# Kernel optimization log

Hardware: AMD Instinct MI355X
Metric: run time of the kernel (lower is better)

The kernel has to match this reference:

```python
import jax, jax.numpy as jnp
import numpy as np

N = 8192          # number of candidate boxes
NUM_CLASSES = 80  # COCO-style class count
IOU_THRESHOLD = 0.45


def setup_inputs() -> dict:
    key = jax.random.key(0)
    k1, k2, k3, k4 = jax.random.split(key, 4)
    # valid xyxy boxes: top-left in [0,1000), width/height in [1,101)
    xy = jax.random.uniform(k1, (N, 2)) * 1000.0
    wh = jax.random.uniform(k2, (N, 2)) * 100.0 + 1.0
    boxes = jnp.concatenate([xy, xy + wh], axis=1)            # [N,4]
    scores = jax.random.uniform(k3, (N,))                     # [N], all > 0
    idxs = jax.random.randint(k4, (N,), 0, NUM_CLASSES)       # [N] class ids
    return {"boxes": boxes, "scores": scores, "idxs": idxs}


def _nms_keep_mask(boxes, scores, iou_thr):
    """Greedy NMS (torchvision semantics) on a single set of boxes.
    Returns a boolean keep mask in the ORIGINAL box order."""
    n = boxes.shape[0]
    order = jnp.argsort(-scores)          # score-descending priority
    b = boxes[order]                      # [n,4]
    area = (b[:, 2] - b[:, 0]) * (b[:, 3] - b[:, 1])
    lt = jnp.maximum(b[:, None, :2], b[None, :, :2])   # [n,n,2]
    rb = jnp.minimum(b[:, None, 2:], b[None, :, 2:])   # [n,n,2]
    wh = jnp.clip(rb - lt, 0.0)
    inter = wh[..., 0] * wh[..., 1]                    # [n,n]
    iou = inter / (area[:, None] + area[None, :] - inter)
    over = iou > iou_thr                               # [n,n] bool
    lower_priority = jnp.arange(n)

    def body(i, suppressed):
        kept_i = jnp.logical_not(suppressed[i])
        # a kept box suppresses all lower-priority boxes it overlaps too much
        return suppressed | (kept_i & over[i] & (lower_priority > i))

    suppressed = jax.lax.fori_loop(0, n, body, jnp.zeros((n,), bool))
    # scatter keep decisions back to original order
    return jnp.zeros((n,), bool).at[order].set(~suppressed)


def reference(boxes, scores, idxs):
    iou_threshold = IOU_THRESHOLD
    # per-class coordinate offsets make boxes of different classes disjoint,
    # so one global NMS == the per-class NMS loop of the torch module
    max_coordinate = boxes.max()
    offsets = idxs.astype(boxes.dtype) * (max_coordinate + 1.0)
    boxes_for_nms = boxes + offsets[:, None]
    keep_mask = _nms_keep_mask(boxes_for_nms, scores, iou_threshold)
    # suppressed boxes get score 0 (all real scores are > 0), so after the
    # descending sort the kept boxes occupy the leading rows exactly as in
    # the torch module; suppressed boxes pad the tail (fixed output shape).
    scores_after_nms = jnp.where(keep_mask, scores, 0.0)
    inds = jnp.argsort(-scores_after_nms)      # [N] keep indices, score-desc
    sorted_scores = scores_after_nms[inds]
    out_boxes = jnp.concatenate([boxes[inds], sorted_scores[:, None]], axis=-1)
    return (out_boxes, inds)
```

## Files before the change

### kernel.cpp

```cpp
#include <hip/hip_runtime.h>
#include <stdint.h>

#define NBOX 8192
#define NW   128
#define IOU_THR 0.45f
#define NCLS 80
#define SEGCAP 128
#define CLSCAP 256
#define EDGE_LDS 2048
#define TAIL_BLOCKS 8

typedef unsigned long long u64;
typedef unsigned int u32;
typedef unsigned short u16;

__global__ void __launch_bounds__(256) k_pm(const float4* __restrict__ boxes4,
                                            const int* __restrict__ idxs,
                                            const float* __restrict__ scores,
                                            u32* __restrict__ ent,
                                            u32* __restrict__ entCnt,
                                            u16* __restrict__ rank16g) {
    int b = blockIdx.x, t = threadIdx.x;
    if (b < NCLS) {
        __shared__ float4 lb[CLSCAP];
        __shared__ float  la[CLSCAP];
        __shared__ float  ls[CLSCAP];
        __shared__ int    lj[CLSCAP];
        __shared__ float  red[256];
        __shared__ u32    ccnt, lcnt;
        float mx = 0.0f;
        for (int i = t; i < NBOX; i += 256) {
            float4 v = boxes4[i];
            mx = fmaxf(mx, fmaxf(fmaxf(v.x, v.y), fmaxf(v.z, v.w)));
        }
        red[t] = mx;
        __syncthreads();
        for (int s = 128; s > 0; s >>= 1) {
            if (t < s) red[t] = fmaxf(red[t], red[t + s]);
            __syncthreads();
        }
        float mc1 = red[0] + 1.0f;
        float off = (float)b * mc1;
        if (t == 0) { ccnt = 0; lcnt = 0; }
        __syncthreads();
        for (int j = t; j < NBOX; j += 256) {
            if (idxs[j] == b) {
                u32 x = atomicAdd(&ccnt, 1u);
                if (x < CLSCAP) {
                    float4 bx = boxes4[j];
                    bx.x += off; bx.y += off; bx.z += off; bx.w += off;
                    lb[x] = bx;
                    la[x] = (bx.z - bx.x) * (bx.w - bx.y);
                    ls[x] = scores[j];
                    lj[x] = j;
                }
            }
        }
        __syncthreads();
        u32 cnt = min(ccnt, (u32)CLSCAP);
        if ((u32)t < cnt) {
            float4 bv = lb[t];
            float  av = la[t];
            float  sv = ls[t];
            int    jv = lj[t];
            for (u32 u = 0; u < (u32)t; ++u) {
                float4 bu = lb[u];
                float ltx = fmaxf(bu.x, bv.x), lty = fmaxf(bu.y, bv.y);
                float rbx = fminf(bu.z, bv.z), rby = fminf(bu.w, bv.w);
                float wx = fmaxf(rbx - ltx, 0.0f), wy = fmaxf(rby - lty, 0.0f);
                float inter = wx * wy;
                if (inter > 0.0f) {
                    float iou = inter / (la[u] + av - inter);
                    if (iou > IOU_THR) {
                        float su = ls[u];
                        int   iu = lj[u];
                        bool uwin = (su > sv) || (su == sv && iu < jv);
                        u32 winI  = uwin ? (u32)iu : (u32)jv;
                        u32 loseI = uwin ? (u32)jv : (u32)iu;
                        u32 x = atomicAdd(&lcnt, 1u);
                        if (x < SEGCAP) ent[b * SEGCAP + x] = (loseI << 13) | winI;
                    }
                }
            }
        }
        __syncthreads();
        if (t == 0) entCnt[b] = min(lcnt, (u32)SEGCAP);
    } else {
        __shared__ u64 lk[2048];
        __shared__ u16 part[256];
        int rb = b - NCLS;
        int jj = rb * 32 + (t & 31);
        u64 kj = ((u64)(~__float_as_uint(scores[jj])) << 32) | (u32)jj;
        int cnt = 0;
        int p = t >> 5;
        for (int ch = 0; ch < 4; ++ch) {
            for (int i = t; i < 2048; i += 256) {
                int g = ch * 2048 + i;
                lk[i] = ((u64)(~__float_as_uint(scores[g])) << 32) | (u32)g;
            }
            __syncthreads();
            int base = p * 256;
#pragma unroll 8
            for (int i = 0; i < 256; ++i) cnt += (lk[base + i] < kj) ? 1 : 0;
            __syncthreads();
        }
        part[t] = (u16)cnt;
        __syncthreads();
        if (t < 32) {
            int s = 0;
#pragma unroll
            for (int q = 0; q < 8; ++q) s += part[q * 32 + t];
            rank16g[rb * 32 + t] = (u16)s;
        }
    }
}

__global__ void __launch_bounds__(1024)
k_tail(const u32* __restrict__ ent, const u32* __restrict__ entCnt,
       const u16* __restrict__ rank16g, const float4* __restrict__ boxes4,
       const float* __restrict__ scores, float* __restrict__ out) {
    __shared__ u32 sedge[EDGE_LDS];
    __shared__ u16 rank16[NBOX];
    __shared__ u32 scnt[NCLS];
    __shared__ u64 kw[NW], sup[NW], kws[NW];
    __shared__ u32 wps[NW], wpo[NW];
    __shared__ u32 s_m, s_nk;
    __shared__ int chg;

    int t = threadIdx.x;
    if (t < NCLS) scnt[t] = entCnt[t];
    for (int j = t; j < NBOX; j += 1024) rank16[j] = rank16g[j];
    if (t < NW) { kw[t] = ~0ULL; kws[t] = 0ULL; }
    if (t == 0) s_m = 0;
    __syncthreads();
    for (u32 idx = t; idx < NCLS * SEGCAP; idx += 1024) {
        u32 seg = idx >> 7, l = idx & 127u;
        if (l < scnt[seg]) {
            u32 pos = atomicAdd(&s_m, 1u);
            if (pos < (u32)EDGE_LDS) sedge[pos] = ent[idx];
        }
    }
    __syncthreads();
    u32 n = min(s_m, (u32)EDGE_LDS);

    for (int iter = 0; iter < NBOX; ++iter) {
        if (t < NW) sup[t] = 0ULL;
        if (t == 0) chg = 0;
        __syncthreads();
        for (u32 e = t; e < n; e += 1024) {
            u32 ed = sedge[e];
            u32 winI = ed & 8191u, loseI = ed >> 13;
            if ((kw[winI >> 6] >> (winI & 63u)) & 1ULL)
                atomicOr(&sup[loseI >> 6], 1ULL << (loseI & 63u));
        }
        __syncthreads();
        if (t < NW) {
            u64 nk2 = ~sup[t];
            if (nk2 != kw[t]) { kw[t] = nk2; chg = 1; }
        }
        __syncthreads();
        int dn = !chg;
        __syncthreads();
        if (dn) break;
    }

    for (int j = t; j < NBOX; j += 1024) {
        if ((kw[j >> 6] >> (j & 63)) & 1ULL) {
            u32 r = rank16[j];
            atomicOr(&kws[r >> 6], 1ULL << (r & 63u));
        }
    }
    __syncthreads();
    if (t < 64) {
        int l = t;
        u32 a0 = (u32)__popcll(kws[2 * l]), a1 = (u32)__popcll(kws[2 * l + 1]);
        u32 s = a0 + a1;
        for (int d = 1; d < 64; d <<= 1) { u32 v = __shfl_up(s, d, 64); if (l >= d) s += v; }
        u32 ex = s - a0 - a1;
        wps[2 * l] = ex; wps[2 * l + 1] = ex + a0;
        if (l == 63) s_nk = s;
        u32 b0 = (u32)__popcll(kw[2 * l]), b1 = (u32)__popcll(kw[2 * l + 1]);
        u32 so = b0 + b1;
        for (int d = 1; d < 64; d <<= 1) { u32 v = __shfl_up(so, d, 64); if (l >= d) so += v; }
        u32 exo = so - b0 - b1;
        wpo[2 * l] = exo; wpo[2 * l + 1] = exo + b0;
    }
    __syncthreads();
    u32 nk = s_nk;

    int j = blockIdx.x * 1024 + t;
    if (j < NBOX) {
        bool kept = (kw[j >> 6] >> (j & 63)) & 1ULL;
        u32 pos;
        if (kept) {
            u32 r = rank16[j];
            pos = wps[r >> 6] + (u32)__popcll(kws[r >> 6] & ((1ULL << (r & 63)) - 1ULL));
        } else {
            u32 prefO = wpo[j >> 6] + (u32)__popcll(kw[j >> 6] & ((1ULL << (j & 63)) - 1ULL));
            pos = nk + (u32)j - prefO;
        }
        float4 bx = boxes4[j];
        float s = kept ? scores[j] : 0.0f;
        out[pos * 5 + 0] = bx.x;
        out[pos * 5 + 1] = bx.y;
        out[pos * 5 + 2] = bx.z;
        out[pos * 5 + 3] = bx.w;
        out[pos * 5 + 4] = s;
        out[NBOX * 5 + pos] = (float)j;
    }
}

extern "C" void kernel_launch(void* const* d_in, const int* in_sizes, int n_in,
                              void* d_out, int out_size, void* d_ws, size_t ws_size,
                              hipStream_t stream) {
    const float* boxes  = (const float*)d_in[0];
    const float* scores = (const float*)d_in[1];
    const int*   idxs   = (const int*)d_in[2];
    float* out = (float*)d_out;

    char* w = (char*)d_ws;
    u32* ent    = (u32*)(w + 0);
    u16* rank16 = (u16*)(w + 40960);
    u32* entCnt = (u32*)(w + 57344);

    k_pm<<<NCLS + 256, 256, 0, stream>>>((const float4*)boxes, idxs, scores, ent, entCnt, rank16);
    k_tail<<<TAIL_BLOCKS, 1024, 0, stream>>>(ent, entCnt, rank16, (const float4*)boxes,
                                             scores, out);
}
```

Before: 45.73 us.

## Compute kept-box output rank in tail kernel instead of global score sort

Drops the 256 rank-computing blocks from the first kernel and stops precomputing a full score rank of all boxes. The tail kernel now launches 256 blocks, each redoing the edge-list fixpoint, and computes each kept box's position by counting kept boxes with higher score (ties broken by index) using wavefront reductions over scores staged in LDS. This shortens the first kernel and removes the rank buffer round trip. In exchange, every tail block repeats the suppression iteration and the score load, and does a 128-step scan per pair of boxes.

```diff
diff --git a/kernel.cpp b/kernel.cpp
--- a/kernel.cpp
+++ b/kernel.cpp
@@ -8,129 +8,105 @@
 #define SEGCAP 128
 #define CLSCAP 256
 #define EDGE_LDS 2048
-#define TAIL_BLOCKS 8
+#define OUTB 256
+#define JPB  32
 
 typedef unsigned long long u64;
 typedef unsigned int u32;
-typedef unsigned short u16;
 
 __global__ void __launch_bounds__(256) k_pm(const float4* __restrict__ boxes4,
                                             const int* __restrict__ idxs,
                                             const float* __restrict__ scores,
                                             u32* __restrict__ ent,
-                                            u32* __restrict__ entCnt,
-                                            u16* __restrict__ rank16g) {
+                                            u32* __restrict__ entCnt) {
     int b = blockIdx.x, t = threadIdx.x;
-    if (b < NCLS) {
-        __shared__ float4 lb[CLSCAP];
-        __shared__ float  la[CLSCAP];
-        __shared__ float  ls[CLSCAP];
-        __shared__ int    lj[CLSCAP];
-        __shared__ float  red[256];
-        __shared__ u32    ccnt, lcnt;
-        float mx = 0.0f;
-        for (int i = t; i < NBOX; i += 256) {
-            float4 v = boxes4[i];
-            mx = fmaxf(mx, fmaxf(fmaxf(v.x, v.y), fmaxf(v.z, v.w)));
-        }
-        red[t] = mx;
-        __syncthreads();
-        for (int s = 128; s > 0; s >>= 1) {
-            if (t < s) red[t] = fmaxf(red[t], red[t + s]);
-            __syncthreads();
-        }
-        float mc1 = red[0] + 1.0f;
-        float off = (float)b * mc1;
-        if (t == 0) { ccnt = 0; lcnt = 0; }
-        __syncthreads();
-        for (int j = t; j < NBOX; j += 256) {
-            if (idxs[j] == b) {
-                u32 x = atomicAdd(&ccnt, 1u);
-                if (x < CLSCAP) {
-                    float4 bx = boxes4[j];
-                    bx.x += off; bx.y += off; bx.z += off; bx.w += off;
-                    lb[x] = bx;
-                    la[x] = (bx.z - bx.x) * (bx.w - bx.y);
-                    ls[x] = scores[j];
-                    lj[x] = j;
+    __shared__ float4 lb[CLSCAP];
+    __shared__ float  la[CLSCAP];
+    __shared__ float  ls[CLSCAP];
+    __shared__ int    lj[CLSCAP];
+    __shared__ float  red[256];
+    __shared__ u32    ccnt, lcnt;
+    float mx = 0.0f;
+    for (int i = t; i < NBOX; i += 256) {
+        float4 v = boxes4[i];
+        mx = fmaxf(mx, fmaxf(fmaxf(v.x, v.y), fmaxf(v.z, v.w)));
+    }
+    red[t] = mx;
+    __syncthreads();
+    for (int s = 128; s > 0; s >>= 1) {
+        if (t < s) red[t] = fmaxf(red[t], red[t + s]);
+        __syncthreads();
+    }
+    float mc1 = red[0] + 1.0f;
+    float off = (float)b * mc1;
+    if (t == 0) { ccnt = 0; lcnt = 0; }
+    __syncthreads();
+    for (int j = t; j < NBOX; j += 256) {
+        if (idxs[j] == b) {
+            u32 x = atomicAdd(&ccnt, 1u);
+            if (x < CLSCAP) {
+                float4 bx = boxes4[j];
+                bx.x += off; bx.y += off; bx.z += off; bx.w += off;
+                lb[x] = bx;
+                la[x] = (bx.z - bx.x) * (bx.w - bx.y);
+                ls[x] = scores[j];
+                lj[x] = j;
+            }
+        }
+    }
+    __syncthreads();
+    u32 cnt = min(ccnt, (u32)CLSCAP);
+    if ((u32)t < cnt) {
+        float4 bv = lb[t];
+        float  av = la[t];
+        float  sv = ls[t];
+        int    jv = lj[t];
+        for (u32 u = 0; u < (u32)t; ++u) {
+            float4 bu = lb[u];
+            float ltx = fmaxf(bu.x, bv.x), lty = fmaxf(bu.y, bv.y);
+            float rbx = fminf(bu.z, bv.z), rby = fminf(bu.w, bv.w);
+            float wx = fmaxf(rbx - ltx, 0.0f), wy = fmaxf(rby - lty, 0.0f);
+            float inter = wx * wy;
+            if (inter > 0.0f) {
+                float iou = inter / (la[u] + av - inter);
+                if (iou > IOU_THR) {
+                    float su = ls[u];
+                    int   iu = lj[u];
+                    bool uwin = (su > sv) || (su == sv && iu < jv);
+                    u32 winI  = uwin ? (u32)iu : (u32)jv;
+                    u32 loseI = uwin ? (u32)jv : (u32)iu;
+                    u32 x = atomicAdd(&lcnt, 1u);
+                    if (x < SEGCAP) ent[b * SEGCAP + x] = (loseI << 13) | winI;
                 }
             }
         }
-        __syncthreads();
-        u32 cnt = min(ccnt, (u32)CLSCAP);
-        if ((u32)t < cnt) {
-            float4 bv = lb[t];
-            float  av = la[t];
-            float  sv = ls[t];
-            int    jv = lj[t];
-            for (u32 u = 0; u < (u32)t; ++u) {
-                float4 bu = lb[u];
-                float ltx = fmaxf(bu.x, bv.x), lty = fmaxf(bu.y, bv.y);
-                float rbx = fminf(bu.z, bv.z), rby = fminf(bu.w, bv.w);
-                float wx = fmaxf(rbx - ltx, 0.0f), wy = fmaxf(rby - lty, 0.0f);
-                float inter = wx * wy;
-                if (inter > 0.0f) {
-                    float iou = inter / (la[u] + av - inter);
-                    if (iou > IOU_THR) {
-                        float su = ls[u];
-                        int   iu = lj[u];
-                        bool uwin = (su > sv) || (su == sv && iu < jv);
-                        u32 winI  = uwin ? (u32)iu : (u32)jv;
-                        u32 loseI = uwin ? (u32)jv : (u32)iu;
-                        u32 x = atomicAdd(&lcnt, 1u);
-                        if (x < SEGCAP) ent[b * SEGCAP + x] = (loseI << 13) | winI;
-                    }
-                }
-            }
-        }
-        __syncthreads();
-        if (t == 0) entCnt[b] = min(lcnt, (u32)SEGCAP);
-    } else {
-        __shared__ u64 lk[2048];
-        __shared__ u16 part[256];
-        int rb = b - NCLS;
-        int jj = rb * 32 + (t & 31);
-        u64 kj = ((u64)(~__float_as_uint(scores[jj])) << 32) | (u32)jj;
-        int cnt = 0;
-        int p = t >> 5;
-        for (int ch = 0; ch < 4; ++ch) {
-            for (int i = t; i < 2048; i += 256) {
-                int g = ch * 2048 + i;
-                lk[i] = ((u64)(~__float_as_uint(scores[g])) << 32) | (u32)g;
-            }
-            __syncthreads();
-            int base = p * 256;
-#pragma unroll 8
-            for (int i = 0; i < 256; ++i) cnt += (lk[base + i] < kj) ? 1 : 0;
-            __syncthreads();
-        }
-        part[t] = (u16)cnt;
-        __syncthreads();
-        if (t < 32) {
-            int s = 0;
-#pragma unroll
-            for (int q = 0; q < 8; ++q) s += part[q * 32 + t];
-            rank16g[rb * 32 + t] = (u16)s;
-        }
-    }
+    }
+    __syncthreads();
+    if (t == 0) entCnt[b] = min(lcnt, (u32)SEGCAP);
 }
 
 __global__ void __launch_bounds__(1024)
 k_tail(const u32* __restrict__ ent, const u32* __restrict__ entCnt,
-       const u16* __restrict__ rank16g, const float4* __restrict__ boxes4,
-       const float* __restrict__ scores, float* __restrict__ out) {
+       const float4* __restrict__ boxes4, const float* __restrict__ scores,
+       float* __restrict__ out) {
+    __shared__ float ssc[NBOX];
     __shared__ u32 sedge[EDGE_LDS];
-    __shared__ u16 rank16[NBOX];
     __shared__ u32 scnt[NCLS];
-    __shared__ u64 kw[NW], sup[NW], kws[NW];
-    __shared__ u32 wps[NW], wpo[NW];
+    __shared__ u64 kw[NW], sup[NW];
+    __shared__ u32 wpo[NW];
+    __shared__ u32 cntj[JPB];
     __shared__ u32 s_m, s_nk;
     __shared__ int chg;
 
     int t = threadIdx.x;
+    const float4* sc4 = (const float4*)scores;
+    for (int q = t; q < NBOX / 4; q += 1024) {
+        float4 v = sc4[q];
+        ssc[q * 4 + 0] = v.x; ssc[q * 4 + 1] = v.y;
+        ssc[q * 4 + 2] = v.z; ssc[q * 4 + 3] = v.w;
+    }
     if (t < NCLS) scnt[t] = entCnt[t];
-    for (int j = t; j < NBOX; j += 1024) rank16[j] = rank16g[j];
-    if (t < NW) { kw[t] = ~0ULL; kws[t] = 0ULL; }
+    if (t < NW) kw[t] = ~0ULL;
     if (t == 0) s_m = 0;
     __syncthreads();
     for (u32 idx = t; idx < NCLS * SEGCAP; idx += 1024) {
@@ -164,43 +140,48 @@
         if (dn) break;
     }
 
-    for (int j = t; j < NBOX; j += 1024) {
-        if ((kw[j >> 6] >> (j & 63)) & 1ULL) {
-            u32 r = rank16[j];
-            atomicOr(&kws[r >> 6], 1ULL << (r & 63u));
-        }
-    }
-    __syncthreads();
     if (t < 64) {
-        int l = t;
-        u32 a0 = (u32)__popcll(kws[2 * l]), a1 = (u32)__popcll(kws[2 * l + 1]);
-        u32 s = a0 + a1;
-        for (int d = 1; d < 64; d <<= 1) { u32 v = __shfl_up(s, d, 64); if (l >= d) s += v; }
-        u32 ex = s - a0 - a1;
-        wps[2 * l] = ex; wps[2 * l + 1] = ex + a0;
-        if (l == 63) s_nk = s;
-        u32 b0 = (u32)__popcll(kw[2 * l]), b1 = (u32)__popcll(kw[2 * l + 1]);
+        u32 b0 = (u32)__popcll(kw[2 * t]), b1 = (u32)__popcll(kw[2 * t + 1]);
         u32 so = b0 + b1;
-        for (int d = 1; d < 64; d <<= 1) { u32 v = __shfl_up(so, d, 64); if (l >= d) so += v; }
+        for (int d = 1; d < 64; d <<= 1) { u32 v = __shfl_up(so, d, 64); if (t >= d) so += v; }
         u32 exo = so - b0 - b1;
-        wpo[2 * l] = exo; wpo[2 * l + 1] = exo + b0;
+        wpo[2 * t] = exo; wpo[2 * t + 1] = exo + b0;
+        if (t == 63) s_nk = so;
     }
     __syncthreads();
     u32 nk = s_nk;
 
-    int j = blockIdx.x * 1024 + t;
-    if (j < NBOX) {
+    int wv = t >> 6, lane = t & 63;
+    int j0 = blockIdx.x * JPB + wv * 2;
+    float s0 = ssc[j0], s1 = ssc[j0 + 1];
+    u32 c0 = 0, c1 = 0;
+    for (int st = 0; st < NW; ++st) {
+        float si = ssc[st * 64 + lane];
+        u64 w = kw[st];
+        u32 kept = (u32)((w >> lane) & 1ULL);
+        int i = st * 64 + lane;
+        c0 += kept & ((u32)(si > s0) | ((u32)(si == s0) & (u32)(i < j0)));
+        c1 += kept & ((u32)(si > s1) | ((u32)(si == s1) & (u32)(i < j0 + 1)));
+    }
+    for (int d = 32; d > 0; d >>= 1) {
+        c0 += __shfl_down(c0, d, 64);
+        c1 += __shfl_down(c1, d, 64);
+    }
+    if (lane == 0) { cntj[wv * 2] = c0; cntj[wv * 2 + 1] = c1; }
+    __syncthreads();
+
+    if (t < JPB) {
+        int j = blockIdx.x * JPB + t;
         bool kept = (kw[j >> 6] >> (j & 63)) & 1ULL;
         u32 pos;
         if (kept) {
-            u32 r = rank16[j];
-            pos = wps[r >> 6] + (u32)__popcll(kws[r >> 6] & ((1ULL << (r & 63)) - 1ULL));
+            pos = cntj[t];
         } else {
             u32 prefO = wpo[j >> 6] + (u32)__popcll(kw[j >> 6] & ((1ULL << (j & 63)) - 1ULL));
             pos = nk + (u32)j - prefO;
         }
         float4 bx = boxes4[j];
-        float s = kept ? scores[j] : 0.0f;
+        float s = kept ? ssc[j] : 0.0f;
         out[pos * 5 + 0] = bx.x;
         out[pos * 5 + 1] = bx.y;
         out[pos * 5 + 2] = bx.z;
@@ -220,10 +201,8 @@
 
     char* w = (char*)d_ws;
     u32* ent    = (u32*)(w + 0);
-    u16* rank16 = (u16*)(w + 40960);
-    u32* entCnt = (u32*)(w + 57344);
-
-    k_pm<<<NCLS + 256, 256, 0, stream>>>((const float4*)boxes, idxs, scores, ent, entCnt, rank16);
-    k_tail<<<TAIL_BLOCKS, 1024, 0, stream>>>(ent, entCnt, rank16, (const float4*)boxes,
-                                             scores, out);
+    u32* entCnt = (u32*)(w + 40960);
+
+    k_pm<<<NCLS, 256, 0, stream>>>((const float4*)boxes, idxs, scores, ent, entCnt);
+    k_tail<<<OUTB, 1024, 0, stream>>>(ent, entCnt, (const float4*)boxes, scores, out);
 }
```

After: 53.97 us. +18.0%, slower.

## Register-block rank computation: each thread compares its keys against 32 target keys

Applied to the files above, without the earlier changes.

The rank blocks no longer stage every score key into LDS and scan it per target. Each thread now loads 32 of the keys directly from global memory and compares each one against the block's 32 target keys, which are held in registers. Per-target counts are then reduced with wave shuffles and combined across the four waves. This removes the LDS traffic and the per-chunk barriers, at the cost of many more live registers and 32 shuffle reductions per thread.

```diff
diff --git a/kernel.cpp b/kernel.cpp
--- a/kernel.cpp
+++ b/kernel.cpp
@@ -86,32 +86,40 @@
         __syncthreads();
         if (t == 0) entCnt[b] = min(lcnt, (u32)SEGCAP);
     } else {
-        __shared__ u64 lk[2048];
-        __shared__ u16 part[256];
+        __shared__ u64 jkl[32];
+        __shared__ u32 part[4][32];
         int rb = b - NCLS;
-        int jj = rb * 32 + (t & 31);
-        u64 kj = ((u64)(~__float_as_uint(scores[jj])) << 32) | (u32)jj;
-        int cnt = 0;
-        int p = t >> 5;
-        for (int ch = 0; ch < 4; ++ch) {
-            for (int i = t; i < 2048; i += 256) {
-                int g = ch * 2048 + i;
-                lk[i] = ((u64)(~__float_as_uint(scores[g])) << 32) | (u32)g;
-            }
-            __syncthreads();
-            int base = p * 256;
-#pragma unroll 8
-            for (int i = 0; i < 256; ++i) cnt += (lk[base + i] < kj) ? 1 : 0;
-            __syncthreads();
-        }
-        part[t] = (u16)cnt;
-        __syncthreads();
         if (t < 32) {
-            int s = 0;
-#pragma unroll
-            for (int q = 0; q < 8; ++q) s += part[q * 32 + t];
-            rank16g[rb * 32 + t] = (u16)s;
-        }
+            int jj = rb * 32 + t;
+            jkl[t] = ((u64)(~__float_as_uint(scores[jj])) << 32) | (u32)jj;
+        }
+        __syncthreads();
+        u64 jk[32];
+#pragma unroll
+        for (int q = 0; q < 32; ++q) jk[q] = jkl[q];
+        u32 cnt[32];
+#pragma unroll
+        for (int q = 0; q < 32; ++q) cnt[q] = 0;
+        for (int q = 0; q < 32; ++q) {
+            int i = q * 256 + t;
+            u64 ik = ((u64)(~__float_as_uint(scores[i])) << 32) | (u32)i;
+#pragma unroll
+            for (int jj = 0; jj < 32; ++jj) cnt[jj] += (u32)(ik < jk[jj]);
+        }
+#pragma unroll
+        for (int jj = 0; jj < 32; ++jj) {
+            u32 c = cnt[jj];
+            for (int d = 1; d < 64; d <<= 1) c += __shfl_xor(c, d, 64);
+            cnt[jj] = c;
+        }
+        int wv = t >> 6;
+        if ((t & 63) == 0) {
+#pragma unroll
+            for (int jj = 0; jj < 32; ++jj) part[wv][jj] = cnt[jj];
+        }
+        __syncthreads();
+        if (t < 32)
+            rank16g[rb * 32 + t] = (u16)(part[0][t] + part[1][t] + part[2][t] + part[3][t]);
     }
 }
 
```

Result: no change. 45.42 us (-0.7%).
